# Performance work log

Measured on AMD Instinct MI355X. Metric: run time of the kernel, lower is better.

Reference implementation:

```python
import jax, jax.numpy as jnp
import numpy as np

DIM = 512; NH = 8; HD = DIM // NH; WS = 28; N = WS * WS; H3 = (DIM * 4) // 3; EPS = 1e-6; B = 16


def _rel_pos_index(H, W):
    # static numpy computation of Swin-style relative position index [N, N]
    coords = np.stack(np.meshgrid(np.arange(H), np.arange(W), indexing='ij')).reshape(2, -1)
    rel = (coords[:, :, None] - coords[:, None, :]).transpose(1, 2, 0)
    rel[..., 0] += H - 1
    rel[..., 1] += W - 1
    rel[..., 0] *= 2 * W - 1
    return rel.sum(-1)

RPI = jnp.asarray(_rel_pos_index(WS, WS))  # [N, N] int


def adaptive_ln(x, w, b, a1w, a1b, a2w, a2b):
    # x: [B,C,H,W]; adapt params from global-avg-pooled 1x1 convs (== matmuls)
    C = x.shape[1]
    pooled = x.mean(axis=(2, 3))                      # [B,C]
    h = jax.nn.relu(pooled @ a1w.T + a1b)             # [B,C/4]
    ad = h @ a2w.T + a2b                              # [B,2C]
    aw = ad[:, :C][:, :, None, None]
    ab = ad[:, C:][:, :, None, None]
    u = x.mean(axis=1, keepdims=True)
    s = ((x - u) ** 2).mean(axis=1, keepdims=True)
    xn = (x - u) * jax.lax.rsqrt(s + EPS)
    return (w[None, :, None, None] * (1.0 + aw)) * xn + (b[None, :, None, None] + ab)


def dwconv(x, w, b):
    y = jax.lax.conv_general_dilated(x, w, (1, 1), 'SAME', feature_group_count=x.shape[1],
                                     dimension_numbers=('NCHW', 'OIHW', 'NCHW'))
    return y + b[None, :, None, None]


def conv1x1(x, w, b):
    return jnp.einsum('bchw,oc->bohw', x, w) + b[None, :, None, None]


def _forward(x, face_priors, n1_w, n1_b, n1_a1w, n1_a1b, n1_a2w, n1_a2b,
             n2_w, n2_b, n2_a1w, n2_a1b, n2_a2w, n2_a2b,
             qkv_w, qkv_b, rpb_table, struct_prior, proj_w, proj_b,
             eye_w, eye_b, nose_w, nose_b, mouth_w, mouth_b,
             fusion_w, fusion_b, gate1_w, gate1_b, gate2_w, gate2_b,
             es1_w, es1_b, es2_w, es2_b, em1_w, em1_b, em2_w, em2_b,
             el1_w, el1_b, el2_w, el2_b, router_w, router_b):
    Bx, C, H, W = x.shape
    n = H * W
    shortcut = x
    xa = adaptive_ln(x, n1_w, n1_b, n1_a1w, n1_a1b, n1_a2w, n1_a2b)
    # --- TripletFaceAttention ---
    xf = xa.reshape(Bx, C, n).transpose(0, 2, 1)                     # [B,N,C]
    qkv = (xf @ qkv_w.T + qkv_b).reshape(Bx, n, 3, NH, HD).transpose(2, 0, 3, 1, 4)
    q, k, v = qkv[0], qkv[1], qkv[2]                                 # [B,h,N,d]
    attn = jnp.einsum('bhnd,bhmd->bhnm', q, k) * (HD ** -0.5)
    attn = attn + struct_prior                                       # learned structure prior [1,h,N,N]
    rpb = rpb_table[RPI]                                             # [N,N,h]
    attn = attn + jnp.transpose(rpb, (2, 0, 1))[None]                # + relative position bias
    attn = attn * face_priors[:, None]                               # multiplicative face mask
    attn = jax.nn.softmax(attn, axis=-1)
    o = jnp.einsum('bhnm,bhmd->bhnd', attn, v).transpose(0, 2, 1, 3).reshape(Bx, n, C)
    o = o @ proj_w.T + proj_b
    x = shortcut + o.transpose(0, 2, 1).reshape(Bx, C, H, W)
    # --- FaceTokenMixer ---
    xn2 = adaptive_ln(x, n2_w, n2_b, n2_a1w, n2_a1b, n2_a2w, n2_a2b)
    cat = jnp.concatenate([dwconv(xn2, eye_w, eye_b),
                           dwconv(xn2, nose_w, nose_b),
                           dwconv(xn2, mouth_w, mouth_b)], axis=1)   # [B,3C,H,W]
    g = jax.nn.sigmoid(conv1x1(jax.nn.relu(conv1x1(xn2, gate1_w, gate1_b)), gate2_w, gate2_b))
    x = x + conv1x1(cat * g, fusion_w, fusion_b)
    # --- EfficientMLP (3-expert MoE, soft routing) ---
    r = jax.nn.softmax(x.mean(axis=(2, 3)) @ router_w.T + router_b, axis=-1)  # [B,3]
    def expert(w1, b1, w2, b2):
        return conv1x1(jax.nn.gelu(conv1x1(x, w1, b1), approximate=False), w2, b2)
    out = (r[:, 0, None, None, None] * expert(es1_w, es1_b, es2_w, es2_b)
           + r[:, 1, None, None, None] * expert(em1_w, em1_b, em2_w, em2_b)
           + r[:, 2, None, None, None] * expert(el1_w, el1_b, el2_w, el2_b))
    return x + out


def setup_inputs() -> dict:
    ks = iter(jax.random.split(jax.random.key(0), 64))
    def rn(shape, s=0.02):
        return jax.random.normal(next(ks), shape, jnp.float32) * s
    d = {}
    d['x'] = jax.random.normal(next(ks), (B, DIM, WS, WS), jnp.float32)
    d['face_priors'] = jax.random.uniform(next(ks), (B, N, N), jnp.float32)
    for p in ('n1', 'n2'):
        d[p + '_w'] = jnp.ones((DIM,), jnp.float32)
        d[p + '_b'] = jnp.zeros((DIM,), jnp.float32)
        d[p + '_a1w'] = rn((DIM // 4, DIM)); d[p + '_a1b'] = jnp.zeros((DIM // 4,), jnp.float32)
        d[p + '_a2w'] = rn((2 * DIM, DIM // 4)); d[p + '_a2b'] = jnp.zeros((2 * DIM,), jnp.float32)
    d['qkv_w'] = rn((3 * DIM, DIM)); d['qkv_b'] = jnp.zeros((3 * DIM,), jnp.float32)
    d['rpb_table'] = rn(((2 * WS - 1) ** 2, NH))
    d['struct_prior'] = rn((1, NH, N, N))
    d['proj_w'] = rn((DIM, DIM)); d['proj_b'] = jnp.zeros((DIM,), jnp.float32)
    d['eye_w'] = rn((DIM, 1, 3, 3)); d['eye_b'] = jnp.zeros((DIM,), jnp.float32)
    d['nose_w'] = rn((DIM, 1, 5, 5)); d['nose_b'] = jnp.zeros((DIM,), jnp.float32)
    d['mouth_w'] = rn((DIM, 1, 7, 7)); d['mouth_b'] = jnp.zeros((DIM,), jnp.float32)
    d['fusion_w'] = rn((DIM, 3 * DIM)); d['fusion_b'] = jnp.zeros((DIM,), jnp.float32)
    d['gate1_w'] = rn((DIM // 4, DIM)); d['gate1_b'] = jnp.zeros((DIM // 4,), jnp.float32)
    d['gate2_w'] = rn((3 * DIM, DIM // 4)); d['gate2_b'] = jnp.zeros((3 * DIM,), jnp.float32)
    for e in ('es', 'em', 'el'):
        d[e + '1_w'] = rn((H3, DIM)); d[e + '1_b'] = jnp.zeros((H3,), jnp.float32)
        d[e + '2_w'] = rn((DIM, H3)); d[e + '2_b'] = jnp.zeros((DIM,), jnp.float32)
    d['router_w'] = rn((3, DIM)); d['router_b'] = jnp.zeros((3,), jnp.float32)
    return d


def reference(x, face_priors, n1_w, n1_b, n1_a1w, n1_a1b, n1_a2w, n1_a2b,
              n2_w, n2_b, n2_a1w, n2_a1b, n2_a2w, n2_a2b,
              qkv_w, qkv_b, rpb_table, struct_prior, proj_w, proj_b,
              eye_w, eye_b, nose_w, nose_b, mouth_w, mouth_b,
              fusion_w, fusion_b, gate1_w, gate1_b, gate2_w, gate2_b,
              es1_w, es1_b, es2_w, es2_b, em1_w, em1_b, em2_w, em2_b,
              el1_w, el1_b, el2_w, el2_b, router_w, router_b):
    return _forward(x, face_priors, n1_w, n1_b, n1_a1w, n1_a1b, n1_a2w, n1_a2b,
                    n2_w, n2_b, n2_a1w, n2_a1b, n2_a2w, n2_a2b,
                    qkv_w, qkv_b, rpb_table, struct_prior, proj_w, proj_b,
                    eye_w, eye_b, nose_w, nose_b, mouth_w, mouth_b,
                    fusion_w, fusion_b, gate1_w, gate1_b, gate2_w, gate2_b,
                    es1_w, es1_b, es2_w, es2_b, em1_w, em1_b, em2_w, em2_b,
                    el1_w, el1_b, el2_w, el2_b, router_w, router_b)
```

## Files before the change

kernel.cpp:

```cpp
#include <hip/hip_runtime.h>
#include <math.h>


#define NPIX 784
#define CDIM 512
#define NHEAD 8
#define C3 1536
#define MTOT 12544

typedef unsigned int uint;
typedef unsigned short ushort;
typedef float f32x4 __attribute__((ext_vector_type(4)));
typedef __bf16 bf16x8 __attribute__((ext_vector_type(8)));

#define OFF_XPM ((size_t)0)
#define OFF_W   ((size_t)3211264)
#define OFF_R2  ((size_t)5324288)
#define OFF_VBF ((size_t)14958080)
#define OFF_OBF ((size_t)18169344)
#define OFF_X2  ((size_t)21380608)
#define OFF_X3  ((size_t)27803136)
#define OFF_PL  ((size_t)34225664)
#define OFF_AD  ((size_t)34233856)
#define OFF_RB  ((size_t)34250240)
#define OFF_US  ((size_t)34250288)
#define OFF_RS  ((size_t)34262832)

#define WOFF_QKV 0
#define WOFF_PROJ 786432
#define WOFF_G1  1048576
#define WOFF_G2  1114112
#define WOFF_FUS 1310720
#define WOFF_E1  2097152
#define WOFF_E2  3144704

__device__ __forceinline__ ushort f2bf(float f) {
  unsigned u = __builtin_bit_cast(unsigned, f);
  unsigned r = (u + 0x7fffu + ((u >> 16) & 1u)) >> 16;
  return (ushort)r;
}
__device__ __forceinline__ unsigned pack2bf(float lo, float hi) {
  return (unsigned)f2bf(lo) | ((unsigned)f2bf(hi) << 16);
}
__device__ __forceinline__ float bf2f(ushort u) {
  unsigned x = ((unsigned)u) << 16;
  return __builtin_bit_cast(float, x);
}
__device__ __forceinline__ void unpack4bf(uint2 v, float* o) {
  o[0] = bf2f((ushort)(v.x & 0xffffu)); o[1] = bf2f((ushort)(v.x >> 16));
  o[2] = bf2f((ushort)(v.y & 0xffffu)); o[3] = bf2f((ushort)(v.y >> 16));
}

__global__ __launch_bounds__(64) void pool_mean_k(const float* __restrict__ x,
                                                  float* __restrict__ pooled) {
  int c = blockIdx.x, b = blockIdx.y;
  const float* row = x + ((size_t)b * CDIM + c) * NPIX;
  float s = 0.f;
  for (int i = threadIdx.x; i < NPIX; i += 64) s += row[i];
  #pragma unroll
  for (int off = 32; off; off >>= 1) s += __shfl_down(s, off);
  if (threadIdx.x == 0) pooled[b * CDIM + c] = s * (1.f / NPIX);
}

__global__ __launch_bounds__(256) void adapt_mlp_k(const float* __restrict__ pooled,
                                                   const float* __restrict__ a1w,
                                                   const float* __restrict__ a1b,
                                                   const float* __restrict__ a2w,
                                                   const float* __restrict__ a2b,
                                                   float* __restrict__ ad) {
  int b = blockIdx.x, tid = threadIdx.x;
  __shared__ float pl[CDIM];
  __shared__ float hh[128];
  for (int i = tid; i < CDIM; i += 256) pl[i] = pooled[b * CDIM + i];
  __syncthreads();
  if (tid < 128) {
    const float* w = a1w + (size_t)tid * CDIM;
    float a = a1b[tid];
    for (int k = 0; k < CDIM; ++k) a += w[k] * pl[k];
    hh[tid] = fmaxf(a, 0.f);
  }
  __syncthreads();
  for (int o = tid; o < 1024; o += 256) {
    const float* w = a2w + (size_t)o * 128;
    float a = a2b[o];
    for (int k = 0; k < 128; ++k) a += w[k] * hh[k];
    ad[b * 1024 + o] = a;
  }
}

template <int STATS>
__global__ __launch_bounds__(256) void ln_pm_k(const float* __restrict__ x,
                                               const float* __restrict__ w,
                                               const float* __restrict__ bias,
                                               const float* __restrict__ ad,
                                               ushort* __restrict__ out,
                                               float* __restrict__ ust,
                                               float* __restrict__ rstp) {
  int b = blockIdx.y;
  int p0 = blockIdx.x * 32;
  int tid = threadIdx.x;
  int px = tid & 31, cg = tid >> 5;
  int p = p0 + px;
  bool valid = p < NPIX;
  const float* xb = x + (size_t)b * CDIM * NPIX;
  float s = 0.f, s2 = 0.f;
  if (valid) {
    for (int c = cg * 64; c < cg * 64 + 64; ++c) {
      float v = xb[(size_t)c * NPIX + p];
      s += v; s2 += v * v;
    }
  }
  __shared__ float rs[8][32], rq[8][32], us[32], vs[32];
  rs[cg][px] = s; rq[cg][px] = s2;
  __syncthreads();
  if (tid < 32) {
    float ts = 0.f, ts2 = 0.f;
    #pragma unroll
    for (int g = 0; g < 8; ++g) { ts += rs[g][tid]; ts2 += rq[g][tid]; }
    float u = ts * (1.f / CDIM);
    float var = ts2 * (1.f / CDIM) - u * u;
    float rv = rsqrtf(var + 1e-6f);
    us[tid] = u; vs[tid] = rv;
    if (STATS && p0 + tid < NPIX) {
      ust[(size_t)b * NPIX + p0 + tid] = u;
      rstp[(size_t)b * NPIX + p0 + tid] = rv;
    }
  }
  __syncthreads();
  if (valid) {
    float u = us[px], rv = vs[px];
    const float* aw = ad + (size_t)b * 1024;
    const float* ab = aw + CDIM;
    ushort* ob = out + ((size_t)(b * NPIX + p)) * CDIM + cg * 64;
    for (int cb = 0; cb < 64; cb += 8) {
      int c = cg * 64 + cb;
      float vv[8];
      #pragma unroll
      for (int q = 0; q < 8; ++q) {
        float v = xb[(size_t)(c + q) * NPIX + p];
        vv[q] = w[c + q] * (1.f + aw[c + q]) * ((v - u) * rv) + (bias[c + q] + ab[c + q]);
      }
      uint4 o = {pack2bf(vv[0], vv[1]), pack2bf(vv[2], vv[3]),
                 pack2bf(vv[4], vv[5]), pack2bf(vv[6], vv[7])};
      *(uint4*)(ob + cb) = o;
    }
  }
}

struct CvtDesc {
  const float* s[11];
  ushort* d[11];
  int rows[11], sk[11], dk[11];
};
__global__ __launch_bounds__(256) void cvt_w_k(CvtDesc D) {
  int seg = blockIdx.y;
  int sk = D.sk[seg], dk = D.dk[seg];
  int total = D.rows[seg] * dk;
  const float* s = D.s[seg];
  ushort* d = D.d[seg];
  for (int i = blockIdx.x * 256 + threadIdx.x; i < total; i += gridDim.x * 256) {
    int r = i / dk, cc = i - r * dk;
    d[i] = (cc < sk) ? f2bf(s[(size_t)r * sk + cc]) : (ushort)0;
  }
}

__global__ __launch_bounds__(256) void sprpb_k(const float* __restrict__ sp,
                                               const float* __restrict__ rpb,
                                               ushort* __restrict__ out) {
  const int q = blockIdx.x, h = blockIdx.y;
  const int i1 = q / 28, j1 = q - i1 * 28;
  const float* src = sp + ((size_t)h * NPIX + q) * NPIX;
  ushort* dst = out + ((size_t)h * NPIX + q) * NPIX;
  for (int m = threadIdx.x; m < NPIX; m += 256) {
    int i2 = m / 28, j2 = m - i2 * 28;
    float rv = rpb[(size_t)((i1 - i2 + 27) * 55 + (j1 - j2 + 27)) * NHEAD + h];
    dst[m] = f2bf(src[m] + rv);
  }
}

__global__ __launch_bounds__(256) void fpcvt_k(const float* __restrict__ fp,
                                               ushort* __restrict__ out) {
  size_t i = (size_t)blockIdx.x * 256 + threadIdx.x;
  float4 v = *((const float4*)fp + i);
  ushort4 o;
  o.x = f2bf(v.x); o.y = f2bf(v.y); o.z = f2bf(v.z); o.w = f2bf(v.w);
  *((ushort4*)out + i) = o;
}

template <int ORIENT, int EPI>
__global__ __launch_bounds__(256) void mgemm_k(const ushort* __restrict__ X,
                                               const ushort* __restrict__ Wt,
                                               const float* __restrict__ bias,
                                               const float* __restrict__ resid,
                                               const float* __restrict__ scales,
                                               void* __restrict__ OutV,
                                               int Ks, int Nreal, int Nstore) {
  const int bid = blockIdx.x;
  const int xcd = bid & 7;
  const int i = bid >> 3;
  const int mt_local = i % 14;
  const int nt = i / 14;
  const int m0 = (xcd * 14 + mt_local) * 112;
  const int n0 = nt * 128;
  const int t = threadIdx.x;
  const int w = t >> 6, lane = t & 63, c = lane & 15, g = lane >> 4;
  __shared__ ushort Xs[7168];
  __shared__ ushort Ws[8192];
  f32x4 acc[7][2];
  #pragma unroll
  for (int mi = 0; mi < 7; ++mi)
    #pragma unroll
    for (int ni = 0; ni < 2; ++ni) acc[mi][ni] = (f32x4){0.f, 0.f, 0.f, 0.f};

  for (int k0 = 0; k0 < Ks; k0 += 64) {
    for (int ii = t; ii < 896; ii += 256) {
      int m = ii >> 3, kg = ii & 7;
      uint4 v = *(const uint4*)(X + (size_t)(m0 + m) * Ks + k0 + kg * 8);
      *(uint4*)&Xs[m * 64 + ((kg ^ (m & 7)) << 3)] = v;
    }
    for (int ii = t; ii < 1024; ii += 256) {
      int n = ii >> 3, kg = ii & 7;
      uint4 v = {0u, 0u, 0u, 0u};
      if (n0 + n < Nreal) v = *(const uint4*)(Wt + (size_t)(n0 + n) * Ks + k0 + kg * 8);
      *(uint4*)&Ws[n * 64 + ((kg ^ (n & 7)) << 3)] = v;
    }
    __syncthreads();
    #pragma unroll
    for (int kc = 0; kc < 2; ++kc) {
      bf16x8 xf[7], wf[2];
      #pragma unroll
      for (int mi = 0; mi < 7; ++mi) {
        int m = mi * 16 + c;
        xf[mi] = *(const bf16x8*)&Xs[m * 64 + (((kc * 4 + g) ^ (m & 7)) << 3)];
      }
      #pragma unroll
      for (int ni = 0; ni < 2; ++ni) {
        int n = w * 32 + ni * 16 + c;
        wf[ni] = *(const bf16x8*)&Ws[n * 64 + (((kc * 4 + g) ^ (n & 7)) << 3)];
      }
      #pragma unroll
      for (int mi = 0; mi < 7; ++mi)
        #pragma unroll
        for (int ni = 0; ni < 2; ++ni)
          acc[mi][ni] = (ORIENT == 0)
            ? __builtin_amdgcn_mfma_f32_16x16x32_bf16(wf[ni], xf[mi], acc[mi][ni], 0, 0, 0)
            : __builtin_amdgcn_mfma_f32_16x16x32_bf16(xf[mi], wf[ni], acc[mi][ni], 0, 0, 0);
    }
    __syncthreads();
  }

  if (ORIENT == 0) {
    ushort* Ob = (ushort*)OutV;
    const int nbq = n0 + w * 32;
    float bi[2][4];
    #pragma unroll
    for (int ni = 0; ni < 2; ++ni)
      #pragma unroll
      for (int j = 0; j < 4; ++j) {
        int n = nbq + ni * 16 + g * 4 + j;
        bi[ni][j] = (n < Nreal) ? bias[n] : 0.f;
      }
    #pragma unroll
    for (int mi = 0; mi < 7; ++mi) {
      int m = m0 + mi * 16 + c;
      #pragma unroll
      for (int ni = 0; ni < 2; ++ni) {
        int nb = nbq + ni * 16 + g * 4;
        if (nb >= Nstore) continue;
        float v[4];
        #pragma unroll
        for (int j = 0; j < 4; ++j) v[j] = acc[mi][ni][j] + bi[ni][j];
        if (EPI == 1) {
          #pragma unroll
          for (int j = 0; j < 4; ++j) v[j] = fmaxf(v[j], 0.f);
        } else if (EPI == 2) {
          #pragma unroll
          for (int j = 0; j < 4; ++j)
            v[j] = 0.5f * v[j] * (1.f + erff(v[j] * 0.70710678118654752f));
        } else if (EPI == 3) {
          uint2 cm = *(const uint2*)&Ob[(size_t)m * Nstore + nb];
          float cf[4];
          unpack4bf(cm, cf);
          #pragma unroll
          for (int j = 0; j < 4; ++j)
            v[j] = (1.f / (1.f + __expf(-v[j]))) * cf[j];
        }
        uint2 o = {pack2bf(v[0], v[1]), pack2bf(v[2], v[3])};
        *(uint2*)&Ob[(size_t)m * Nstore + nb] = o;
      }
    }
  } else {
    const int bb = m0 / NPIX;
    const int prow = m0 - bb * NPIX;
    float* Ob = (float*)OutV + (size_t)bb * CDIM * NPIX;
    const float* Rb = resid + (size_t)bb * CDIM * NPIX;
    float sc = scales ? scales[bb * 3] : 1.f;
    #pragma unroll
    for (int ni = 0; ni < 2; ++ni) {
      int n = n0 + w * 32 + ni * 16 + c;
      float bv = bias[n];
      #pragma unroll
      for (int mi = 0; mi < 7; ++mi) {
        int p = prow + mi * 16 + g * 4;
        size_t off = (size_t)n * NPIX + p;
        float4 r = *(const float4*)&Rb[off];
        f32x4 a = acc[mi][ni];
        float4 o = {r.x + sc * (a[0] + bv), r.y + sc * (a[1] + bv),
                    r.z + sc * (a[2] + bv), r.w + sc * (a[3] + bv)};
        *(float4*)&Ob[off] = o;
      }
    }
  }
}

__global__ __launch_bounds__(256) void vtr_k(const ushort* __restrict__ qkvbf,
                                             ushort* __restrict__ vbf) {
  const int p0 = blockIdx.x * 64, c0 = blockIdx.y * 64, b = blockIdx.z;
  __shared__ ushort T[64][72];
  for (int idx = threadIdx.x; idx < 512; idx += 256) {
    int pl = idx >> 3, cq = idx & 7;
    int p = p0 + pl;
    uint4 v = {0u, 0u, 0u, 0u};
    if (p < NPIX)
      v = *(const uint4*)(qkvbf + (size_t)(b * NPIX + p) * C3 + 1024 + c0 + cq * 8);
    *(uint4*)&T[pl][cq * 8] = v;
  }
  __syncthreads();
  for (int idx = threadIdx.x; idx < 512; idx += 256) {
    int cl = idx >> 3, pq = idx & 7;
    if (p0 + pq * 8 < NPIX) {
      ushort tmp[8];
      #pragma unroll
      for (int i = 0; i < 8; ++i) tmp[i] = T[pq * 8 + i][cl];
      *(uint4*)(vbf + ((size_t)(b * CDIM + c0 + cl)) * NPIX + p0 + pq * 8) =
          *(const uint4*)&tmp[0];
    }
  }
}

__global__ __launch_bounds__(256) void tr_cvt_k(const float* __restrict__ src,
                                                ushort* __restrict__ dst) {
  const int p0 = blockIdx.x * 64, c0 = blockIdx.y * 64, b = blockIdx.z;
  __shared__ ushort T[64][72];
  const float* sb = src + (size_t)b * CDIM * NPIX;
  for (int idx = threadIdx.x; idx < 4096; idx += 256) {
    int ci = idx >> 6, pj = idx & 63;
    int p = p0 + pj;
    T[pj][ci] = (p < NPIX) ? f2bf(sb[(size_t)(c0 + ci) * NPIX + p]) : (ushort)0;
  }
  __syncthreads();
  for (int idx = threadIdx.x; idx < 512; idx += 256) {
    int pj = idx >> 3, cq = idx & 7;
    int p = p0 + pj;
    if (p < NPIX) {
      uint4 v = *(const uint4*)&T[pj][cq * 8];
      *(uint4*)(dst + ((size_t)(b * NPIX + p)) * CDIM + c0 + cq * 8) = v;
    }
  }
}

__global__ __launch_bounds__(256) void attn_mfma_k(const ushort* __restrict__ qkvbf,
                                                   const ushort* __restrict__ vbf,
                                                   const ushort* __restrict__ sprpb,
                                                   const ushort* __restrict__ fpb,
                                                   ushort* __restrict__ obf) {
  const int bid = blockIdx.x;
  const int xcd = bid & 7;
  const int i = bid >> 3;
  const int b = xcd + 8 * (i / 56);
  const int r = i % 56;
  const int h = r & 7;
  const int qt = r >> 3;
  const int w = threadIdx.x >> 6, lane = threadIdx.x & 63;
  const int g = lane >> 4, c = lane & 15;
  const int q0 = qt * 128 + w * 32;
  if (q0 >= NPIX) return;
  const bool hasB = (q0 + 16) < NPIX;
  const int qA = q0 + c;
  const int qB = q0 + 16 + c;

  __shared__ uint BL[4][2][384];
  uint* bwA = BL[w][0];
  uint* bwB = BL[w][1];

  const ushort* qpA = qkvbf + (size_t)(b * NPIX + qA) * C3 + h * 64 + g * 8;
  const bf16x8 qfA0 = *(const bf16x8*)qpA;
  const bf16x8 qfA1 = *(const bf16x8*)(qpA + 32);
  bf16x8 qfB0 = qfA0, qfB1 = qfA1;
  if (hasB) {
    const ushort* qpB = qkvbf + (size_t)(b * NPIX + qB) * C3 + h * 64 + g * 8;
    qfB0 = *(const bf16x8*)qpB;
    qfB1 = *(const bf16x8*)(qpB + 32);
  }

  const ushort* kbase = qkvbf + (size_t)b * NPIX * C3 + 512 + h * 64 + g * 8;
  const ushort* vbase = vbf + ((size_t)b * CDIM + h * 64) * NPIX;
  const ushort* sprA = sprpb + ((size_t)h * NPIX + qA) * NPIX;
  const ushort* sprB = sprpb + ((size_t)h * NPIX + (hasB ? qB : qA)) * NPIX;
  const ushort* fpA = fpb + ((size_t)b * NPIX + qA) * NPIX;
  const ushort* fpB = fpb + ((size_t)b * NPIX + (hasB ? qB : qA)) * NPIX;

  f32x4 oA0 = {0.f, 0.f, 0.f, 0.f}, oA1 = oA0, oA2 = oA0, oA3 = oA0;
  f32x4 oB0 = oA0, oB1 = oA0, oB2 = oA0, oB3 = oA0;
  float MA = -1e30f, LA = 0.f, MB = -1e30f, LB = 0.f;

  for (int ms = 0; ms < 25; ++ms) {
    const int m0 = ms * 32;
    const bool full = (ms < 24);

    const ushort* kp = kbase + (size_t)(m0 + c) * C3;
    bf16x8 ka0 = *(const bf16x8*)kp;
    bf16x8 ka1 = *(const bf16x8*)(kp + 32);
    bf16x8 kb0 = ka0, kb1 = ka1;
    if (full) {
      const ushort* kp1 = kp + (size_t)16 * C3;
      kb0 = *(const bf16x8*)kp1;
      kb1 = *(const bf16x8*)(kp1 + 32);
    }

    f32x4 sA0 = {0.f, 0.f, 0.f, 0.f}, sA1 = sA0;
    sA0 = __builtin_amdgcn_mfma_f32_16x16x32_bf16(ka0, qfA0, sA0, 0, 0, 0);
    sA0 = __builtin_amdgcn_mfma_f32_16x16x32_bf16(ka1, qfA1, sA0, 0, 0, 0);
    if (full) {
      sA1 = __builtin_amdgcn_mfma_f32_16x16x32_bf16(kb0, qfA0, sA1, 0, 0, 0);
      sA1 = __builtin_amdgcn_mfma_f32_16x16x32_bf16(kb1, qfA1, sA1, 0, 0, 0);
    }

    float vA0[4], vA1[4];
    {
      float spv[4], fpv[4];
      unpack4bf(*(const uint2*)(sprA + m0 + g * 4), spv);
      unpack4bf(*(const uint2*)(fpA + m0 + g * 4), fpv);
      #pragma unroll
      for (int j = 0; j < 4; ++j) vA0[j] = fmaf(sA0[j], 0.125f, spv[j]) * fpv[j];
      if (full) {
        unpack4bf(*(const uint2*)(sprA + m0 + 16 + g * 4), spv);
        unpack4bf(*(const uint2*)(fpA + m0 + 16 + g * 4), fpv);
        #pragma unroll
        for (int j = 0; j < 4; ++j) vA1[j] = fmaf(sA1[j], 0.125f, spv[j]) * fpv[j];
      }
    }
    {
      float tm = fmaxf(fmaxf(vA0[0], vA0[1]), fmaxf(vA0[2], vA0[3]));
      if (full) tm = fmaxf(tm, fmaxf(fmaxf(vA1[0], vA1[1]), fmaxf(vA1[2], vA1[3])));
      tm = fmaxf(tm, __shfl_xor(tm, 16));
      tm = fmaxf(tm, __shfl_xor(tm, 32));
      const float nM = fmaxf(MA, tm);
      const float fac = __expf(MA - nM);
      float p0v[4], p1v[4];
      float ps = 0.f;
      #pragma unroll
      for (int j = 0; j < 4; ++j) { p0v[j] = __expf(vA0[j] - nM); ps += p0v[j]; }
      if (full) {
        #pragma unroll
        for (int j = 0; j < 4; ++j) { p1v[j] = __expf(vA1[j] - nM); ps += p1v[j]; }
      }
      ps += __shfl_xor(ps, 16);
      ps += __shfl_xor(ps, 32);
      LA = LA * fac + ps;
      MA = nM;
      #pragma unroll
      for (int j = 0; j < 4; ++j) { oA0[j] *= fac; oA1[j] *= fac; oA2[j] *= fac; oA3[j] *= fac; }
      uint2 wlo, whi;
      wlo.x = pack2bf(p0v[0], p0v[1]);
      wlo.y = pack2bf(p0v[2], p0v[3]);
      whi.x = full ? pack2bf(p1v[0], p1v[1]) : 0u;
      whi.y = full ? pack2bf(p1v[2], p1v[3]) : 0u;
      *(uint2*)&bwA[lane * 6] = wlo;
      *(uint2*)&bwA[lane * 6 + 2] = whi;
    }

    if (hasB) {
      f32x4 sB0 = {0.f, 0.f, 0.f, 0.f}, sB1 = sB0;
      sB0 = __builtin_amdgcn_mfma_f32_16x16x32_bf16(ka0, qfB0, sB0, 0, 0, 0);
      sB0 = __builtin_amdgcn_mfma_f32_16x16x32_bf16(ka1, qfB1, sB0, 0, 0, 0);
      if (full) {
        sB1 = __builtin_amdgcn_mfma_f32_16x16x32_bf16(kb0, qfB0, sB1, 0, 0, 0);
        sB1 = __builtin_amdgcn_mfma_f32_16x16x32_bf16(kb1, qfB1, sB1, 0, 0, 0);
      }
      float vB0[4], vB1[4];
      {
        float spv[4], fpv[4];
        unpack4bf(*(const uint2*)(sprB + m0 + g * 4), spv);
        unpack4bf(*(const uint2*)(fpB + m0 + g * 4), fpv);
        #pragma unroll
        for (int j = 0; j < 4; ++j) vB0[j] = fmaf(sB0[j], 0.125f, spv[j]) * fpv[j];
        if (full) {
          unpack4bf(*(const uint2*)(sprB + m0 + 16 + g * 4), spv);
          unpack4bf(*(const uint2*)(fpB + m0 + 16 + g * 4), fpv);
          #pragma unroll
          for (int j = 0; j < 4; ++j) vB1[j] = fmaf(sB1[j], 0.125f, spv[j]) * fpv[j];
        }
      }
      float tm = fmaxf(fmaxf(vB0[0], vB0[1]), fmaxf(vB0[2], vB0[3]));
      if (full) tm = fmaxf(tm, fmaxf(fmaxf(vB1[0], vB1[1]), fmaxf(vB1[2], vB1[3])));
      tm = fmaxf(tm, __shfl_xor(tm, 16));
      tm = fmaxf(tm, __shfl_xor(tm, 32));
      const float nM = fmaxf(MB, tm);
      const float fac = __expf(MB - nM);
      float p0v[4], p1v[4];
      float ps = 0.f;
      #pragma unroll
      for (int j = 0; j < 4; ++j) { p0v[j] = __expf(vB0[j] - nM); ps += p0v[j]; }
      if (full) {
        #pragma unroll
        for (int j = 0; j < 4; ++j) { p1v[j] = __expf(vB1[j] - nM); ps += p1v[j]; }
      }
      ps += __shfl_xor(ps, 16);
      ps += __shfl_xor(ps, 32);
      LB = LB * fac + ps;
      MB = nM;
      #pragma unroll
      for (int j = 0; j < 4; ++j) { oB0[j] *= fac; oB1[j] *= fac; oB2[j] *= fac; oB3[j] *= fac; }
      uint2 wlo, whi;
      wlo.x = pack2bf(p0v[0], p0v[1]);
      wlo.y = pack2bf(p0v[2], p0v[3]);
      whi.x = full ? pack2bf(p1v[0], p1v[1]) : 0u;
      whi.y = full ? pack2bf(p1v[2], p1v[3]) : 0u;
      *(uint2*)&bwB[lane * 6] = wlo;
      *(uint2*)&bwB[lane * 6 + 2] = whi;
    }

    const int f = g >> 1;
    const int slo = 32 * (g & 1) + c;
    uint2 blo = *(const uint2*)&bwA[slo * 6 + f * 2];
    uint2 bhi = *(const uint2*)&bwA[(slo + 16) * 6 + f * 2];
    uint4 bba = {blo.x, blo.y, bhi.x, bhi.y};
    const bf16x8 pfA = __builtin_bit_cast(bf16x8, bba);

    const ushort* vp = vbase + (size_t)c * NPIX + m0 + g * 8;
    bf16x8 vf0 = *(const bf16x8*)(vp);
    bf16x8 vf1 = *(const bf16x8*)(vp + (size_t)16 * NPIX);
    bf16x8 vf2 = *(const bf16x8*)(vp + (size_t)32 * NPIX);
    bf16x8 vf3 = *(const bf16x8*)(vp + (size_t)48 * NPIX);
    oA0 = __builtin_amdgcn_mfma_f32_16x16x32_bf16(vf0, pfA, oA0, 0, 0, 0);
    oA1 = __builtin_amdgcn_mfma_f32_16x16x32_bf16(vf1, pfA, oA1, 0, 0, 0);
    oA2 = __builtin_amdgcn_mfma_f32_16x16x32_bf16(vf2, pfA, oA2, 0, 0, 0);
    oA3 = __builtin_amdgcn_mfma_f32_16x16x32_bf16(vf3, pfA, oA3, 0, 0, 0);
    if (hasB) {
      uint2 clo = *(const uint2*)&bwB[slo * 6 + f * 2];
      uint2 chi = *(const uint2*)&bwB[(slo + 16) * 6 + f * 2];
      uint4 bbb = {clo.x, clo.y, chi.x, chi.y};
      const bf16x8 pfB = __builtin_bit_cast(bf16x8, bbb);
      oB0 = __builtin_amdgcn_mfma_f32_16x16x32_bf16(vf0, pfB, oB0, 0, 0, 0);
      oB1 = __builtin_amdgcn_mfma_f32_16x16x32_bf16(vf1, pfB, oB1, 0, 0, 0);
      oB2 = __builtin_amdgcn_mfma_f32_16x16x32_bf16(vf2, pfB, oB2, 0, 0, 0);
      oB3 = __builtin_amdgcn_mfma_f32_16x16x32_bf16(vf3, pfB, oB3, 0, 0, 0);
    }
  }

  {
    const float invL = 1.f / LA;
    ushort* dst = obf + (size_t)(b * NPIX + qA) * CDIM + h * 64 + g * 4;
    f32x4 ot[4] = {oA0, oA1, oA2, oA3};
    #pragma unroll
    for (int t2 = 0; t2 < 4; ++t2) {
      uint2 o = {pack2bf(ot[t2][0] * invL, ot[t2][1] * invL),
                 pack2bf(ot[t2][2] * invL, ot[t2][3] * invL)};
      *(uint2*)(dst + t2 * 16) = o;
    }
  }
  if (hasB) {
    const float invL = 1.f / LB;
    ushort* dst = obf + (size_t)(b * NPIX + qB) * CDIM + h * 64 + g * 4;
    f32x4 ot[4] = {oB0, oB1, oB2, oB3};
    #pragma unroll
    for (int t2 = 0; t2 < 4; ++t2) {
      uint2 o = {pack2bf(ot[t2][0] * invL, ot[t2][1] * invL),
                 pack2bf(ot[t2][2] * invL, ot[t2][3] * invL)};
      *(uint2*)(dst + t2 * 16) = o;
    }
  }
}

__device__ __forceinline__ float bf2f_s(ushort u) { return bf2f(u); }

template <int R>
__device__ __forceinline__ void conv_pass(const ushort* __restrict__ plane_ci,
                                          const float* __restrict__ wl_ci,
                                          float bv, int slot,
                                          ushort (*__restrict__ outb)[16], int ci) {
  constexpr int K = 2 * R + 1;
  float wreg[K * K];
  #pragma unroll
  for (int i = 0; i < K * K; ++i) wreg[i] = wl_ci[i];
  #pragma unroll
  for (int r7 = 0; r7 < 7; ++r7) {
    const int run = slot + r7 * 16;
    const int y = run >> 2, x0 = (run & 3) * 7;
    float acc[7];
    #pragma unroll
    for (int i = 0; i < 7; ++i) acc[i] = bv;
    #pragma unroll
    for (int dy = 0; dy < K; ++dy) {
      const ushort* rp = plane_ci + (y + 3 - R + dy) * 34 + (x0 + 3 - R);
      float win[7 + 2 * R];
      #pragma unroll
      for (int k = 0; k < 7 + 2 * R; ++k) win[k] = bf2f_s(rp[k]);
      #pragma unroll
      for (int i = 0; i < 7; ++i)
        #pragma unroll
        for (int k = 0; k < K; ++k)
          acc[i] = fmaf(win[i + k], wreg[dy * K + k], acc[i]);
    }
    #pragma unroll
    for (int i = 0; i < 7; ++i) outb[y * 28 + x0 + i][ci] = f2bf(acc[i]);
  }
}

__global__ __launch_bounds__(256) void dwln_k(const float* __restrict__ x2,
    const float* __restrict__ ust, const float* __restrict__ rst,
    const float* __restrict__ ad, const float* __restrict__ n2w,
    const float* __restrict__ n2b,
    const float* __restrict__ ew, const float* __restrict__ eb,
    const float* __restrict__ nw, const float* __restrict__ nb,
    const float* __restrict__ mw, const float* __restrict__ mb,
    ushort* __restrict__ cat) {
  const int cg = blockIdx.x, b = blockIdx.y;
  const int c0 = cg * 16;
  const int t = threadIdx.x;
  const int ci = t & 15, slot = t >> 4;

  __shared__ ushort plane[16][1156];
  __shared__ ushort outb[784][16];
  __shared__ float Wl[16 * 49];
  __shared__ float LWs[16], LBs[16];

  {
    uint* pz = (uint*)&plane[0][0];
    for (int i = t; i < 16 * 1156 / 2; i += 256) pz[i] = 0u;
  }
  if (t < 16) {
    int cc = c0 + t;
    float aw = ad[b * 1024 + cc], ab = ad[b * 1024 + 512 + cc];
    LWs[t] = n2w[cc] * (1.f + aw);
    LBs[t] = n2b[cc] + ab;
  }
  __syncthreads();

  {
    float uu[4], rr[4];
    #pragma unroll
    for (int j = 0; j < 4; ++j) {
      int p = t + j * 256;
      if (p < NPIX) {
        uu[j] = ust[(size_t)b * NPIX + p];
        rr[j] = rst[(size_t)b * NPIX + p];
      }
    }
    for (int cc = 0; cc < 16; ++cc) {
      const float* xp = x2 + ((size_t)(b * CDIM + c0 + cc)) * NPIX;
      float lw = LWs[cc], lb = LBs[cc];
      #pragma unroll
      for (int j = 0; j < 4; ++j) {
        int p = t + j * 256;
        if (p < NPIX) {
          int y = p / 28, xx2 = p - y * 28;
          plane[cc][(y + 3) * 34 + xx2 + 3] = f2bf(lw * (xp[p] - uu[j]) * rr[j] + lb);
        }
      }
    }
  }
  __syncthreads();

  #pragma unroll 1
  for (int cv = 0; cv < 3; ++cv) {
    const float* gw = (cv == 0) ? ew : (cv == 1) ? nw : mw;
    const float* gb = (cv == 0) ? eb : (cv == 1) ? nb : mb;
    const int K2 = (cv == 0) ? 9 : (cv == 1) ? 25 : 49;
    for (int i = t; i < 16 * K2; i += 256) {
      int cc = i / K2, k = i - cc * K2;
      Wl[cc * K2 + k] = gw[(size_t)(c0 + cc) * K2 + k];
    }
    __syncthreads();
    float bv = gb[c0 + ci];
    if (cv == 0)      conv_pass<1>(&plane[ci][0], &Wl[ci * 9],  bv, slot, outb, ci);
    else if (cv == 1) conv_pass<2>(&plane[ci][0], &Wl[ci * 25], bv, slot, outb, ci);
    else              conv_pass<3>(&plane[ci][0], &Wl[ci * 49], bv, slot, outb, ci);
    __syncthreads();
    for (int idx = t; idx < NPIX * 2; idx += 256) {
      int p = idx >> 1, half = idx & 1;
      uint4 v = *(const uint4*)&outb[p][half * 8];
      *(uint4*)(cat + ((size_t)(b * NPIX + p)) * C3 + cv * 512 + c0 + half * 8) = v;
    }
    __syncthreads();
  }
}

__global__ __launch_bounds__(64) void router_k(const float* __restrict__ pooled,
                                               const float* __restrict__ rw,
                                               const float* __restrict__ rb,
                                               float* __restrict__ r) {
  int b = blockIdx.x, lane = threadIdx.x;
  float a0 = 0.f, a1 = 0.f, a2 = 0.f;
  for (int k = lane; k < CDIM; k += 64) {
    float p = pooled[b * CDIM + k];
    a0 += rw[k] * p;
    a1 += rw[CDIM + k] * p;
    a2 += rw[2 * CDIM + k] * p;
  }
  #pragma unroll
  for (int off = 32; off; off >>= 1) {
    a0 += __shfl_down(a0, off);
    a1 += __shfl_down(a1, off);
    a2 += __shfl_down(a2, off);
  }
  if (lane == 0) {
    float l0 = a0 + rb[0], l1 = a1 + rb[1], l2 = a2 + rb[2];
    float mx = fmaxf(l0, fmaxf(l1, l2));
    float e0 = __expf(l0 - mx), e1 = __expf(l1 - mx), e2 = __expf(l2 - mx);
    float inv = 1.f / (e0 + e1 + e2);
    r[b * 3 + 0] = e0 * inv;
    r[b * 3 + 1] = e1 * inv;
    r[b * 3 + 2] = e2 * inv;
  }
}

extern "C" void kernel_launch(void* const* d_in, const int* in_sizes, int n_in,
                              void* d_out, int out_size, void* d_ws, size_t ws_size,
                              hipStream_t stream) {
  (void)in_sizes; (void)n_in; (void)out_size; (void)ws_size;
  const float* x         = (const float*)d_in[0];
  const float* fpri      = (const float*)d_in[1];
  const float* n1_w      = (const float*)d_in[2];
  const float* n1_b      = (const float*)d_in[3];
  const float* n1_a1w    = (const float*)d_in[4];
  const float* n1_a1b    = (const float*)d_in[5];
  const float* n1_a2w    = (const float*)d_in[6];
  const float* n1_a2b    = (const float*)d_in[7];
  const float* n2_w      = (const float*)d_in[8];
  const float* n2_b      = (const float*)d_in[9];
  const float* n2_a1w    = (const float*)d_in[10];
  const float* n2_a1b    = (const float*)d_in[11];
  const float* n2_a2w    = (const float*)d_in[12];
  const float* n2_a2b    = (const float*)d_in[13];
  const float* qkv_w     = (const float*)d_in[14];
  const float* qkv_b     = (const float*)d_in[15];
  const float* rpb_table = (const float*)d_in[16];
  const float* sprior    = (const float*)d_in[17];
  const float* proj_w    = (const float*)d_in[18];
  const float* proj_b    = (const float*)d_in[19];
  const float* eye_w     = (const float*)d_in[20];
  const float* eye_b     = (const float*)d_in[21];
  const float* nose_w    = (const float*)d_in[22];
  const float* nose_b    = (const float*)d_in[23];
  const float* mouth_w   = (const float*)d_in[24];
  const float* mouth_b   = (const float*)d_in[25];
  const float* fusion_w  = (const float*)d_in[26];
  const float* fusion_b  = (const float*)d_in[27];
  const float* gate1_w   = (const float*)d_in[28];
  const float* gate1_b   = (const float*)d_in[29];
  const float* gate2_w   = (const float*)d_in[30];
  const float* gate2_b   = (const float*)d_in[31];
  const float* e1w[3] = {(const float*)d_in[32], (const float*)d_in[36], (const float*)d_in[40]};
  const float* e1b[3] = {(const float*)d_in[33], (const float*)d_in[37], (const float*)d_in[41]};
  const float* e2w[3] = {(const float*)d_in[34], (const float*)d_in[38], (const float*)d_in[42]};
  const float* e2b[3] = {(const float*)d_in[35], (const float*)d_in[39], (const float*)d_in[43]};
  const float* router_w  = (const float*)d_in[44];
  const float* router_b  = (const float*)d_in[45];

  float* ws    = (float*)d_ws;
  ushort* xpm  = (ushort*)(ws + OFF_XPM);
  ushort* wb   = (ushort*)(ws + OFF_W);
  ushort* r2u  = (ushort*)(ws + OFF_R2);
  ushort* vbf  = (ushort*)(ws + OFF_VBF);
  ushort* obf  = (ushort*)(ws + OFF_OBF);
  float* x2    = ws + OFF_X2;
  float* x3    = ws + OFF_X3;
  float* pld   = ws + OFF_PL;
  float* adb   = ws + OFF_AD;
  float* rbuf  = ws + OFF_RB;
  float* ust   = ws + OFF_US;
  float* rst   = ws + OFF_RS;
  float* outp  = (float*)d_out;

  ushort* qkvw = wb + WOFF_QKV;
  ushort* projw = wb + WOFF_PROJ;
  ushort* g1w  = wb + WOFF_G1;
  ushort* g2w  = wb + WOFF_G2;
  ushort* fusw = wb + WOFF_FUS;

  ushort* fpbf   = (ushort*)x2;
  ushort* sprpbf = (ushort*)x3;

  CvtDesc D;
  D.s[0] = qkv_w;    D.d[0] = qkvw;  D.rows[0] = 1536; D.sk[0] = 512;  D.dk[0] = 512;
  D.s[1] = proj_w;   D.d[1] = projw; D.rows[1] = 512;  D.sk[1] = 512;  D.dk[1] = 512;
  D.s[2] = gate1_w;  D.d[2] = g1w;   D.rows[2] = 128;  D.sk[2] = 512;  D.dk[2] = 512;
  D.s[3] = gate2_w;  D.d[3] = g2w;   D.rows[3] = 1536; D.sk[3] = 128;  D.dk[3] = 128;
  D.s[4] = fusion_w; D.d[4] = fusw;  D.rows[4] = 512;  D.sk[4] = 1536; D.dk[4] = 1536;
  for (int e = 0; e < 3; ++e) {
    D.s[5 + e] = e1w[e]; D.d[5 + e] = wb + WOFF_E1 + e * 349184;
    D.rows[5 + e] = 682; D.sk[5 + e] = 512; D.dk[5 + e] = 512;
    D.s[8 + e] = e2w[e]; D.d[8 + e] = wb + WOFF_E2 + e * 360448;
    D.rows[8 + e] = 512; D.sk[8 + e] = 682; D.dk[8 + e] = 704;
  }
  cvt_w_k<<<dim3(512, 11), 256, 0, stream>>>(D);

  sprpb_k<<<dim3(NPIX, NHEAD), 256, 0, stream>>>(sprior, rpb_table, sprpbf);
  fpcvt_k<<<9604, 256, 0, stream>>>(fpri, fpbf);

  pool_mean_k<<<dim3(CDIM, 16), 64, 0, stream>>>(x, pld);
  adapt_mlp_k<<<16, 256, 0, stream>>>(pld, n1_a1w, n1_a1b, n1_a2w, n1_a2b, adb);
  ln_pm_k<0><<<dim3(25, 16), 256, 0, stream>>>(x, n1_w, n1_b, adb, xpm, nullptr, nullptr);

  mgemm_k<0, 0><<<1344, 256, 0, stream>>>(xpm, qkvw, qkv_b, nullptr, nullptr,
                                          r2u, 512, 1536, 1536);
  vtr_k<<<dim3(13, 8, 16), 256, 0, stream>>>(r2u, vbf);
  attn_mfma_k<<<896, 256, 0, stream>>>(r2u, vbf, sprpbf, fpbf, obf);
  mgemm_k<1, 4><<<448, 256, 0, stream>>>(obf, projw, proj_b, x, nullptr,
                                         x2, 512, 512, 512);

  pool_mean_k<<<dim3(CDIM, 16), 64, 0, stream>>>(x2, pld);
  adapt_mlp_k<<<16, 256, 0, stream>>>(pld, n2_a1w, n2_a1b, n2_a2w, n2_a2b, adb);
  ln_pm_k<1><<<dim3(25, 16), 256, 0, stream>>>(x2, n2_w, n2_b, adb, xpm, ust, rst);
  dwln_k<<<dim3(32, 16), 256, 0, stream>>>(x2, ust, rst, adb, n2_w, n2_b,
                                           eye_w, eye_b, nose_w, nose_b, mouth_w, mouth_b,
                                           r2u);
  mgemm_k<0, 1><<<112, 256, 0, stream>>>(xpm, g1w, gate1_b, nullptr, nullptr,
                                         obf, 512, 128, 128);
  mgemm_k<0, 3><<<1344, 256, 0, stream>>>(obf, g2w, gate2_b, nullptr, nullptr,
                                          r2u, 128, 1536, 1536);
  mgemm_k<1, 4><<<448, 256, 0, stream>>>(r2u, fusw, fusion_b, x2, nullptr,
                                         x3, 1536, 512, 512);

  tr_cvt_k<<<dim3(13, 8, 16), 256, 0, stream>>>(x3, vbf);
  pool_mean_k<<<dim3(CDIM, 16), 64, 0, stream>>>(x3, pld);
  router_k<<<16, 64, 0, stream>>>(pld, router_w, router_b, rbuf);
  for (int e = 0; e < 3; ++e) {
    mgemm_k<0, 2><<<672, 256, 0, stream>>>(vbf, wb + WOFF_E1 + e * 349184,
                                           e1b[e], nullptr, nullptr,
                                           r2u, 512, 682, 704);
    mgemm_k<1, 4><<<448, 256, 0, stream>>>(r2u, wb + WOFF_E2 + e * 360448,
                                           e2b[e], (e == 0) ? x3 : outp,
                                           rbuf + e, outp, 704, 512, 512);
  }
}
```

Baseline: 862.4 us.

## Fuse three expert MLPs into two concatenated GEMMs and skip redundant softmax rescales

Measured after the change: 816.7 us. 5.3% less time.

```diff
diff --git a/kernel.cpp b/kernel.cpp
--- a/kernel.cpp
+++ b/kernel.cpp
@@ -6,12 +6,12 @@
 #define CDIM 512
 #define NHEAD 8
 #define C3 1536
-#define MTOT 12544
 
 typedef unsigned int uint;
 typedef unsigned short ushort;
 typedef float f32x4 __attribute__((ext_vector_type(4)));
 typedef __bf16 bf16x8 __attribute__((ext_vector_type(8)));
+typedef __bf16 bf16x2 __attribute__((ext_vector_type(2)));
 
 #define OFF_XPM ((size_t)0)
 #define OFF_W   ((size_t)3211264)
@@ -25,6 +25,7 @@
 #define OFF_RB  ((size_t)34250240)
 #define OFF_US  ((size_t)34250288)
 #define OFF_RS  ((size_t)34262832)
+#define OFF_E2C ((size_t)34275392)
 
 #define WOFF_QKV 0
 #define WOFF_PROJ 786432
@@ -32,15 +33,14 @@
 #define WOFF_G2  1114112
 #define WOFF_FUS 1310720
 #define WOFF_E1  2097152
-#define WOFF_E2  3144704
 
 __device__ __forceinline__ ushort f2bf(float f) {
-  unsigned u = __builtin_bit_cast(unsigned, f);
-  unsigned r = (u + 0x7fffu + ((u >> 16) & 1u)) >> 16;
-  return (ushort)r;
+  __bf16 h = (__bf16)f;
+  return __builtin_bit_cast(ushort, h);
 }
 __device__ __forceinline__ unsigned pack2bf(float lo, float hi) {
-  return (unsigned)f2bf(lo) | ((unsigned)f2bf(hi) << 16);
+  bf16x2 v = {(__bf16)lo, (__bf16)hi};
+  return __builtin_bit_cast(unsigned, v);
 }
 __device__ __forceinline__ float bf2f(ushort u) {
   unsigned x = ((unsigned)u) << 16;
@@ -150,17 +150,17 @@
 struct CvtDesc {
   const float* s[11];
   ushort* d[11];
-  int rows[11], sk[11], dk[11];
+  int rows[11], sk[11], dk[11], ds[11], rr[11];
 };
 __global__ __launch_bounds__(256) void cvt_w_k(CvtDesc D) {
   int seg = blockIdx.y;
-  int sk = D.sk[seg], dk = D.dk[seg];
+  int sk = D.sk[seg], dk = D.dk[seg], ds = D.ds[seg], rr = D.rr[seg];
   int total = D.rows[seg] * dk;
   const float* s = D.s[seg];
   ushort* d = D.d[seg];
   for (int i = blockIdx.x * 256 + threadIdx.x; i < total; i += gridDim.x * 256) {
     int r = i / dk, cc = i - r * dk;
-    d[i] = (cc < sk) ? f2bf(s[(size_t)r * sk + cc]) : (ushort)0;
+    d[(size_t)r * ds + cc] = (cc < sk && r < rr) ? f2bf(s[(size_t)r * sk + cc]) : (ushort)0;
   }
 }
 
@@ -185,6 +185,27 @@
   ushort4 o;
   o.x = f2bf(v.x); o.y = f2bf(v.y); o.z = f2bf(v.z); o.w = f2bf(v.w);
   *((ushort4*)out + i) = o;
+}
+
+__global__ __launch_bounds__(512) void biaseff_k(const float* __restrict__ rbuf,
+                                                 const float* __restrict__ b0,
+                                                 const float* __restrict__ b1,
+                                                 const float* __restrict__ b2,
+                                                 const float* __restrict__ a0,
+                                                 const float* __restrict__ a1,
+                                                 const float* __restrict__ a2,
+                                                 float* __restrict__ be,
+                                                 float* __restrict__ e1bcat) {
+  int b = blockIdx.x;
+  if (b < 16) {
+    int n = threadIdx.x;
+    be[b * 512 + n] = rbuf[b * 3] * b0[n] + rbuf[b * 3 + 1] * b1[n] + rbuf[b * 3 + 2] * b2[n];
+  } else {
+    for (int i = threadIdx.x; i < 2112; i += 512) {
+      int e = i / 704, r = i - e * 704;
+      e1bcat[i] = (r < 682) ? (e == 0 ? a0 : e == 1 ? a1 : a2)[r] : 0.f;
+    }
+  }
 }
 
 template <int ORIENT, int EPI>
@@ -202,6 +223,7 @@
   const int nt = i / 14;
   const int m0 = (xcd * 14 + mt_local) * 112;
   const int n0 = nt * 128;
+  const int bb = m0 / NPIX;
   const int t = threadIdx.x;
   const int w = t >> 6, lane = t & 63, c = lane & 15, g = lane >> 4;
   __shared__ ushort Xs[7168];
@@ -284,21 +306,26 @@
           #pragma unroll
           for (int j = 0; j < 4; ++j)
             v[j] = (1.f / (1.f + __expf(-v[j]))) * cf[j];
+        } else if (EPI == 5) {
+          int e = nb / 704; e = (e > 2) ? 2 : e;
+          float sc = scales[bb * 3 + e];
+          #pragma unroll
+          for (int j = 0; j < 4; ++j)
+            v[j] = 0.5f * v[j] * (1.f + erff(v[j] * 0.70710678118654752f)) * sc;
         }
         uint2 o = {pack2bf(v[0], v[1]), pack2bf(v[2], v[3])};
         *(uint2*)&Ob[(size_t)m * Nstore + nb] = o;
       }
     }
   } else {
-    const int bb = m0 / NPIX;
     const int prow = m0 - bb * NPIX;
     float* Ob = (float*)OutV + (size_t)bb * CDIM * NPIX;
     const float* Rb = resid + (size_t)bb * CDIM * NPIX;
-    float sc = scales ? scales[bb * 3] : 1.f;
+    float sc = (EPI == 4 && scales) ? scales[bb * 3] : 1.f;
     #pragma unroll
     for (int ni = 0; ni < 2; ++ni) {
       int n = n0 + w * 32 + ni * 16 + c;
-      float bv = bias[n];
+      float bv = (EPI == 5) ? bias[(size_t)bb * CDIM + n] : bias[n];
       #pragma unroll
       for (int mi = 0; mi < 7; ++mi) {
         int p = prow + mi * 16 + g * 4;
@@ -445,22 +472,25 @@
       if (full) tm = fmaxf(tm, fmaxf(fmaxf(vA1[0], vA1[1]), fmaxf(vA1[2], vA1[3])));
       tm = fmaxf(tm, __shfl_xor(tm, 16));
       tm = fmaxf(tm, __shfl_xor(tm, 32));
-      const float nM = fmaxf(MA, tm);
-      const float fac = __expf(MA - nM);
+      if (__any(tm > MA)) {
+        const float nM = fmaxf(MA, tm);
+        const float fac = __expf(MA - nM);
+        LA *= fac;
+        #pragma unroll
+        for (int j = 0; j < 4; ++j) { oA0[j] *= fac; oA1[j] *= fac; oA2[j] *= fac; oA3[j] *= fac; }
+        MA = nM;
+      }
       float p0v[4], p1v[4];
       float ps = 0.f;
       #pragma unroll
-      for (int j = 0; j < 4; ++j) { p0v[j] = __expf(vA0[j] - nM); ps += p0v[j]; }
+      for (int j = 0; j < 4; ++j) { p0v[j] = __expf(vA0[j] - MA); ps += p0v[j]; }
       if (full) {
         #pragma unroll
-        for (int j = 0; j < 4; ++j) { p1v[j] = __expf(vA1[j] - nM); ps += p1v[j]; }
+        for (int j = 0; j < 4; ++j) { p1v[j] = __expf(vA1[j] - MA); ps += p1v[j]; }
       }
       ps += __shfl_xor(ps, 16);
       ps += __shfl_xor(ps, 32);
-      LA = LA * fac + ps;
-      MA = nM;
-      #pragma unroll
-      for (int j = 0; j < 4; ++j) { oA0[j] *= fac; oA1[j] *= fac; oA2[j] *= fac; oA3[j] *= fac; }
+      LA += ps;
       uint2 wlo, whi;
       wlo.x = pack2bf(p0v[0], p0v[1]);
       wlo.y = pack2bf(p0v[2], p0v[3]);
@@ -496,22 +526,25 @@
       if (full) tm = fmaxf(tm, fmaxf(fmaxf(vB1[0], vB1[1]), fmaxf(vB1[2], vB1[3])));
       tm = fmaxf(tm, __shfl_xor(tm, 16));
       tm = fmaxf(tm, __shfl_xor(tm, 32));
-      const float nM = fmaxf(MB, tm);
-      const float fac = __expf(MB - nM);
+      if (__any(tm > MB)) {
+        const float nM = fmaxf(MB, tm);
+        const float fac = __expf(MB - nM);
+        LB *= fac;
+        #pragma unroll
+        for (int j = 0; j < 4; ++j) { oB0[j] *= fac; oB1[j] *= fac; oB2[j] *= fac; oB3[j] *= fac; }
+        MB = nM;
+      }
       float p0v[4], p1v[4];
       float ps = 0.f;
       #pragma unroll
-      for (int j = 0; j < 4; ++j) { p0v[j] = __expf(vB0[j] - nM); ps += p0v[j]; }
+      for (int j = 0; j < 4; ++j) { p0v[j] = __expf(vB0[j] - MB); ps += p0v[j]; }
       if (full) {
         #pragma unroll
-        for (int j = 0; j < 4; ++j) { p1v[j] = __expf(vB1[j] - nM); ps += p1v[j]; }
+        for (int j = 0; j < 4; ++j) { p1v[j] = __expf(vB1[j] - MB); ps += p1v[j]; }
       }
       ps += __shfl_xor(ps, 16);
       ps += __shfl_xor(ps, 32);
-      LB = LB * fac + ps;
-      MB = nM;
-      #pragma unroll
-      for (int j = 0; j < 4; ++j) { oB0[j] *= fac; oB1[j] *= fac; oB2[j] *= fac; oB3[j] *= fac; }
+      LB += ps;
       uint2 wlo, whi;
       wlo.x = pack2bf(p0v[0], p0v[1]);
       wlo.y = pack2bf(p0v[2], p0v[3]);
@@ -774,26 +807,33 @@
   float* rst   = ws + OFF_RS;
   float* outp  = (float*)d_out;
 
-  ushort* qkvw = wb + WOFF_QKV;
+  ushort* qkvw  = wb + WOFF_QKV;
   ushort* projw = wb + WOFF_PROJ;
-  ushort* g1w  = wb + WOFF_G1;
-  ushort* g2w  = wb + WOFF_G2;
-  ushort* fusw = wb + WOFF_FUS;
+  ushort* g1w   = wb + WOFF_G1;
+  ushort* g2w   = wb + WOFF_G2;
+  ushort* fusw  = wb + WOFF_FUS;
+  ushort* e1cat = wb + WOFF_E1;
+  ushort* e2cat = (ushort*)(ws + OFF_E2C);
+  float* be     = adb;
+  float* e1bcat = adb + 8192;
 
   ushort* fpbf   = (ushort*)x2;
   ushort* sprpbf = (ushort*)x3;
 
   CvtDesc D;
-  D.s[0] = qkv_w;    D.d[0] = qkvw;  D.rows[0] = 1536; D.sk[0] = 512;  D.dk[0] = 512;
-  D.s[1] = proj_w;   D.d[1] = projw; D.rows[1] = 512;  D.sk[1] = 512;  D.dk[1] = 512;
-  D.s[2] = gate1_w;  D.d[2] = g1w;   D.rows[2] = 128;  D.sk[2] = 512;  D.dk[2] = 512;
-  D.s[3] = gate2_w;  D.d[3] = g2w;   D.rows[3] = 1536; D.sk[3] = 128;  D.dk[3] = 128;
-  D.s[4] = fusion_w; D.d[4] = fusw;  D.rows[4] = 512;  D.sk[4] = 1536; D.dk[4] = 1536;
+  auto seg = [&](int s2, const float* src, ushort* dst, int rows, int sk, int dk,
+                 int ds, int rr) {
+    D.s[s2] = src; D.d[s2] = dst; D.rows[s2] = rows; D.sk[s2] = sk;
+    D.dk[s2] = dk; D.ds[s2] = ds; D.rr[s2] = rr;
+  };
+  seg(0, qkv_w,    qkvw,  1536, 512,  512,  512,  1536);
+  seg(1, proj_w,   projw, 512,  512,  512,  512,  512);
+  seg(2, gate1_w,  g1w,   128,  512,  512,  512,  128);
+  seg(3, gate2_w,  g2w,   1536, 128,  128,  128,  1536);
+  seg(4, fusion_w, fusw,  512,  1536, 1536, 1536, 512);
   for (int e = 0; e < 3; ++e) {
-    D.s[5 + e] = e1w[e]; D.d[5 + e] = wb + WOFF_E1 + e * 349184;
-    D.rows[5 + e] = 682; D.sk[5 + e] = 512; D.dk[5 + e] = 512;
-    D.s[8 + e] = e2w[e]; D.d[8 + e] = wb + WOFF_E2 + e * 360448;
-    D.rows[8 + e] = 512; D.sk[8 + e] = 682; D.dk[8 + e] = 704;
+    seg(5 + e, e1w[e], e1cat + (size_t)e * 704 * 512, 704, 512, 512, 512, 682);
+    seg(8 + e, e2w[e], e2cat + (size_t)e * 704,       512, 682, 704, 2112, 512);
   }
   cvt_w_k<<<dim3(512, 11), 256, 0, stream>>>(D);
 
@@ -824,15 +864,13 @@
   mgemm_k<1, 4><<<448, 256, 0, stream>>>(r2u, fusw, fusion_b, x2, nullptr,
                                          x3, 1536, 512, 512);
 
-  tr_cvt_k<<<dim3(13, 8, 16), 256, 0, stream>>>(x3, vbf);
+  tr_cvt_k<<<dim3(13, 8, 16), 256, 0, stream>>>(x3, xpm);
   pool_mean_k<<<dim3(CDIM, 16), 64, 0, stream>>>(x3, pld);
   router_k<<<16, 64, 0, stream>>>(pld, router_w, router_b, rbuf);
-  for (int e = 0; e < 3; ++e) {
-    mgemm_k<0, 2><<<672, 256, 0, stream>>>(vbf, wb + WOFF_E1 + e * 349184,
-                                           e1b[e], nullptr, nullptr,
-                                           r2u, 512, 682, 704);
-    mgemm_k<1, 4><<<448, 256, 0, stream>>>(r2u, wb + WOFF_E2 + e * 360448,
-                                           e2b[e], (e == 0) ? x3 : outp,
-                                           rbuf + e, outp, 704, 512, 512);
-  }
-}
+  biaseff_k<<<17, 512, 0, stream>>>(rbuf, e2b[0], e2b[1], e2b[2],
+                                    e1b[0], e1b[1], e1b[2], be, e1bcat);
+  mgemm_k<0, 5><<<1904, 256, 0, stream>>>(xpm, e1cat, e1bcat, nullptr, rbuf,
+                                          r2u, 512, 2112, 2112);
+  mgemm_k<1, 5><<<448, 256, 0, stream>>>(r2u, e2cat, be, x3, nullptr,
+                                         outp, 2112, 512, 512);
+}
```
